# Optimization experiments

Hardware: AMD Instinct MI355X
Metric: run time of the kernel (lower is better)

The kernel has to match this reference:

```python
import jax, jax.numpy as jnp
import numpy as np

B, N, E, H, DEPTH = 2, 2048, 1024, 8, 12
D = E // H // 2  # head_dim = 64
LN_EPS = 1e-5


def setup_inputs() -> dict:
    key = jax.random.key(0)
    ks = jax.random.split(key, 10)
    w = lambda k: jax.random.normal(k, (E, E), jnp.float32) * (E ** -0.5)
    lp = lambda k: jax.random.normal(k, (D,), jnp.float32) * 0.1
    return {
        "x": jax.random.normal(ks[0], (B, N, E), jnp.float32),
        "Wq": w(ks[1]), "Wk": w(ks[2]), "Wv": w(ks[3]), "Wo": w(ks[4]),
        "lq1": lp(ks[5]), "lk1": lp(ks[6]), "lq2": lp(ks[7]), "lk2": lp(ks[8]),
        "ln_g": jnp.ones((2 * D,), jnp.float32),
        "ln_b": jnp.zeros((2 * D,), jnp.float32),
    }


def reference(x, Wq, Wk, Wv, Wo, lq1, lk1, lq2, lk2, ln_g, ln_b):
    b, n, e = x.shape
    lam_init = 0.8 - 0.6 * np.exp(-0.3 * DEPTH)  # lambda_init_fn(depth)
    # projections; split into 2H half-heads of dim D for q,k; H heads of dim 2D for v
    q = (x @ Wq).reshape(b, n, 2 * H, D).transpose(0, 2, 1, 3) * (D ** -0.5)  # [b,2H,n,D]
    k = (x @ Wk).reshape(b, n, 2 * H, D).transpose(0, 2, 1, 3)                # [b,2H,n,D]
    v = (x @ Wv).reshape(b, n, H, 2 * D).transpose(0, 2, 1, 3)                # [b,H,n,2D]
    scores = jnp.einsum('bhqd,bhkd->bhqk', q, k)                              # [b,2H,n,n]
    attn = jax.nn.softmax(scores, axis=-1).reshape(b, H, 2, n, n)
    lam = jnp.exp(jnp.sum(lq1 * lk1)) - jnp.exp(jnp.sum(lq2 * lk2)) + lam_init
    w_diff = attn[:, :, 0] - lam * attn[:, :, 1]                              # [b,H,n,n]
    o = jnp.einsum('bhqk,bhkd->bhqd', w_diff, v)                              # [b,H,n,2D]
    # per-head LayerNorm over channel dim 2D
    mu = o.mean(-1, keepdims=True)
    var = ((o - mu) ** 2).mean(-1, keepdims=True)
    o = (o - mu) * jax.lax.rsqrt(var + LN_EPS) * ln_g + ln_b
    o = o.transpose(0, 2, 1, 3).reshape(b, n, e)
    return o @ Wo
```

## Files before the change

### kernel.cpp

```cpp
#include <hip/hip_runtime.h>
#include <hip/hip_bf16.h>
#include <math.h>

#define B_ 2
#define N_ 2048
#define E_ 1024
#define H_ 8

typedef __attribute__((ext_vector_type(8))) short frag8;
typedef __attribute__((ext_vector_type(4))) float f32x4;
typedef __attribute__((ext_vector_type(16))) float f32x16;
typedef __attribute__((ext_vector_type(8))) unsigned short u16x8;

constexpr float LAM_INIT = 0.7836057665316245f;
constexpr float LOG2E = 1.4426950408889634f;
constexpr float EXP2_GUARD = -23.083120654f;

static __device__ __forceinline__ float fast_exp2(float x) {
#if __has_builtin(__builtin_amdgcn_exp2f)
  return __builtin_amdgcn_exp2f(x);
#else
  return exp2f(x);
#endif
}

static __device__ __forceinline__ ushort f2bf(float f) {
  union { float f; unsigned u; } v; v.f = f;
  unsigned r = (v.u + 0x7FFFu + ((v.u >> 16) & 1u)) >> 16;
  return (ushort)r;
}

static __device__ __forceinline__ unsigned pkbf(float a, float b) {
  __hip_bfloat162 h = __float22bfloat162_rn(make_float2(a, b));
  return *(unsigned*)&h;
}

static __device__ __forceinline__ float bf2f_lo(unsigned u) {
  union { unsigned u; float f; } v; v.u = u << 16; return v.f;
}
static __device__ __forceinline__ float bf2f_hi(unsigned u) {
  union { unsigned u; float f; } v; v.u = u & 0xFFFF0000u; return v.f;
}

static __device__ __forceinline__ void async16(const void* g, void* l) {
  __builtin_amdgcn_global_load_lds((const __attribute__((address_space(1))) void*)g,
                                   (__attribute__((address_space(3))) void*)l, 16, 0, 0);
}

static __device__ __forceinline__ frag8 mkfrag(unsigned p0, unsigned p1,
                                               unsigned p2, unsigned p3) {
  auto r02 = __builtin_amdgcn_permlane32_swap((int)p0, (int)p2, false, false);
  auto r13 = __builtin_amdgcn_permlane32_swap((int)p1, (int)p3, false, false);
  union { unsigned u[4]; frag8 f; } u;
  u.u[0] = (unsigned)r02[0];
  u.u[1] = (unsigned)r13[0];
  u.u[2] = (unsigned)r02[1];
  u.u[3] = (unsigned)r13[1];
  return u.f;
}

__global__ __launch_bounds__(256) void prep_kernel(
    const float* __restrict__ x,
    const float* __restrict__ Wq, const float* __restrict__ Wk,
    const float* __restrict__ Wv, const float* __restrict__ Wo,
    const float* __restrict__ lq1, const float* __restrict__ lk1,
    const float* __restrict__ lq2, const float* __restrict__ lk2,
    ushort* __restrict__ xb, ushort* __restrict__ wqkvt, ushort* __restrict__ wot,
    float* __restrict__ lam_out) {
  __shared__ ushort t[64][72];
  const int bx = blockIdx.x;
  const int tid = threadIdx.x;
  if (bx < 2048) {
    int i = bx * 256 + tid;
    const float4* sp = (const float4*)x + (size_t)i * 2;
    float4 a = sp[0], b = sp[1];
    u16x8 o;
    o[0] = f2bf(a.x); o[1] = f2bf(a.y); o[2] = f2bf(a.z); o[3] = f2bf(a.w);
    o[4] = f2bf(b.x); o[5] = f2bf(b.y); o[6] = f2bf(b.z); o[7] = f2bf(b.w);
    *(u16x8*)(xb + (size_t)i * 8) = o;
  } else if (bx < 3072) {
    int idx = bx - 2048;
    int sel = idx >> 8, rem = idx & 255;
    const float* W = (sel == 0) ? Wq : (sel == 1) ? Wk : (sel == 2) ? Wv : Wo;
    ushort* Wt = (sel < 3) ? (wqkvt + (size_t)sel * 1048576) : wot;
    const int c0 = (rem & 15) * 64, r0 = (rem >> 4) * 64;
    {
      int r = tid >> 2, cc = (tid & 3) * 16;
      const float* sp = W + (size_t)(r0 + r) * 1024 + c0 + cc;
      #pragma unroll
      for (int j = 0; j < 4; j++) {
        float4 a = *(const float4*)(sp + j * 4);
        t[cc + j * 4 + 0][r] = f2bf(a.x);
        t[cc + j * 4 + 1][r] = f2bf(a.y);
        t[cc + j * 4 + 2][r] = f2bf(a.z);
        t[cc + j * 4 + 3][r] = f2bf(a.w);
      }
    }
    __syncthreads();
    int c = tid >> 2, rr = (tid & 3) * 16;
    ushort* dp = Wt + (size_t)(c0 + c) * 1024 + r0 + rr;
    *(u16x8*)dp = *(u16x8*)&t[c][rr];
    *(u16x8*)(dp + 8) = *(u16x8*)&t[c][rr + 8];
  } else {
    if (tid < 64) {
      float t1 = lq1[tid] * lk1[tid];
      float t2 = lq2[tid] * lk2[tid];
      #pragma unroll
      for (int off = 32; off > 0; off >>= 1) {
        t1 += __shfl_down(t1, off);
        t2 += __shfl_down(t2, off);
      }
      if (tid == 0) lam_out[0] = expf(t1) - expf(t2) + LAM_INIT;
    }
  }
}

__global__ __launch_bounds__(256) void gemm_qkv(const ushort* __restrict__ xb,
                                                const ushort* __restrict__ wqkvt,
                                                ushort* __restrict__ qkb,
                                                ushort* __restrict__ vtb, float qscale) {
  __shared__ ushort As[4096];
  __shared__ ushort Bs[4096];
  const int id = blockIdx.x;
  const ushort* A; const ushort* Bt; ushort* C;
  int m0, n0, ldc;
  float sc;
  if (id < 512) {
    m0 = (id >> 4) * 128; n0 = (id & 15) * 128;
    A = xb; Bt = wqkvt; C = qkb; ldc = 2048;
    sc = (n0 < 1024) ? qscale : 1.0f;
  } else {
    int id2 = id - 512;
    m0 = (id2 & 7) * 128; n0 = (id2 >> 3) * 128;
    A = wqkvt + 2 * 1048576; Bt = xb; C = vtb; ldc = 4096;
    sc = 1.0f;
  }
  const int tid = threadIdx.x;
  const int w = tid >> 6, l = tid & 63;
  const int quad = l >> 4, col16 = l & 15;
  const int wm = (w & 1) * 64, wn = (w >> 1) * 64;
  const int lrow = l >> 2, lcol = (l & 3) * 8;

  f32x4 acc[4][4];
  #pragma unroll
  for (int mt = 0; mt < 4; mt++)
    #pragma unroll
    for (int nt = 0; nt < 4; nt++) acc[mt][nt] = (f32x4){0.f, 0.f, 0.f, 0.f};

  for (int k0 = 0; k0 < 1024; k0 += 32) {
    __syncthreads();
    #pragma unroll
    for (int i = 0; i < 4; i++) {
      int s = w * 4 + i;
      if (s < 8) {
        const ushort* gp = A + (size_t)(m0 + s * 16 + lrow) * 1024 + k0 + lcol;
        async16(gp, (char*)As + s * 1024);
      } else {
        int s2 = s - 8;
        const ushort* gp = Bt + (size_t)(n0 + s2 * 16 + lrow) * 1024 + k0 + lcol;
        async16(gp, (char*)Bs + s2 * 1024);
      }
    }
    __syncthreads();
    frag8 af[4], bfr[4];
    #pragma unroll
    for (int mt = 0; mt < 4; mt++)
      af[mt] = *(const frag8*)((const char*)As + (wm + mt * 16 + col16) * 64 + quad * 16);
    #pragma unroll
    for (int nt = 0; nt < 4; nt++)
      bfr[nt] = *(const frag8*)((const char*)Bs + (wn + nt * 16 + col16) * 64 + quad * 16);
    #pragma unroll
    for (int mt = 0; mt < 4; mt++)
      #pragma unroll
      for (int nt = 0; nt < 4; nt++)
        acc[mt][nt] = __builtin_amdgcn_mfma_f32_16x16x32_bf16(af[mt], bfr[nt], acc[mt][nt], 0, 0, 0);
  }

  #pragma unroll
  for (int mt = 0; mt < 4; mt++)
    #pragma unroll
    for (int r = 0; r < 4; r++) {
      int m = m0 + wm + mt * 16 + quad * 4 + r;
      #pragma unroll
      for (int nt = 0; nt < 4; nt++) {
        int n = n0 + wn + nt * 16 + col16;
        C[(size_t)m * ldc + n] = f2bf(acc[mt][nt][r] * sc);
      }
    }
}

__global__ __launch_bounds__(256) void gemm_out(const ushort* __restrict__ A,
                                                const ushort* __restrict__ Bt,
                                                float* __restrict__ Cp) {
  __shared__ ushort As[2048];
  __shared__ ushort Bs[4096];
  const int tid = threadIdx.x;
  const int w = tid >> 6, l = tid & 63;
  const int quad = l >> 4, col16 = l & 15;
  const int m0 = blockIdx.y * 64, n0 = blockIdx.x * 128;
  const int wm = (w & 1) * 32, wn = (w >> 1) * 64;
  const int lrow = l >> 2, lcol = (l & 3) * 8;

  f32x4 acc[2][4];
  #pragma unroll
  for (int mt = 0; mt < 2; mt++)
    #pragma unroll
    for (int nt = 0; nt < 4; nt++) acc[mt][nt] = (f32x4){0.f, 0.f, 0.f, 0.f};

  for (int k0 = 0; k0 < 1024; k0 += 32) {
    __syncthreads();
    #pragma unroll
    for (int i = 0; i < 3; i++) {
      int s = w * 3 + i;
      if (s < 4) {
        const ushort* gp = A + (size_t)(m0 + s * 16 + lrow) * 1024 + k0 + lcol;
        async16(gp, (char*)As + s * 1024);
      } else {
        int s2 = s - 4;
        const ushort* gp = Bt + (size_t)(n0 + s2 * 16 + lrow) * 1024 + k0 + lcol;
        async16(gp, (char*)Bs + s2 * 1024);
      }
    }
    __syncthreads();
    frag8 af[2], bfr[4];
    #pragma unroll
    for (int mt = 0; mt < 2; mt++)
      af[mt] = *(const frag8*)((const char*)As + (wm + mt * 16 + col16) * 64 + quad * 16);
    #pragma unroll
    for (int nt = 0; nt < 4; nt++)
      bfr[nt] = *(const frag8*)((const char*)Bs + (wn + nt * 16 + col16) * 64 + quad * 16);
    #pragma unroll
    for (int mt = 0; mt < 2; mt++)
      #pragma unroll
      for (int nt = 0; nt < 4; nt++)
        acc[mt][nt] = __builtin_amdgcn_mfma_f32_16x16x32_bf16(af[mt], bfr[nt], acc[mt][nt], 0, 0, 0);
  }

  #pragma unroll
  for (int mt = 0; mt < 2; mt++)
    #pragma unroll
    for (int r = 0; r < 4; r++) {
      int m = m0 + wm + mt * 16 + quad * 4 + r;
      #pragma unroll
      for (int nt = 0; nt < 4; nt++) {
        int n = n0 + wn + nt * 16 + col16;
        Cp[(size_t)m * 1024 + n] = acc[mt][nt][r];
      }
    }
}

__global__ __launch_bounds__(256, 2) void flash_kernel(const ushort* __restrict__ qk,
                                                       const ushort* __restrict__ vt,
                                                       ushort* __restrict__ opart,
                                                       float* __restrict__ lbuf) {
  const int h2 = blockIdx.y;
  const int b = blockIdx.z;
  const int h = h2 >> 1;
  const int tid = threadIdx.x;
  const int w = tid >> 6;
  const int lane31 = tid & 31, half = (tid & 63) >> 5;
  const int i0 = blockIdx.x * 128 + w * 32;

  __shared__ ushort Klds0[64 * 64], Klds1[64 * 64];
  __shared__ ushort Vlds0[128 * 64], Vlds1[128 * 64];

  frag8 qf[4];
  #pragma unroll
  for (int chk = 0; chk < 4; chk++) {
    const ushort* qp = qk + (size_t)(b * N_ + i0 + lane31) * 2048 +
                       h2 * 64 + chk * 16 + half * 8;
    qf[chk] = *(const frag8*)qp;
  }

  f32x16 o_[4];
  #pragma unroll
  for (int cm = 0; cm < 4; cm++)
    #pragma unroll
    for (int i = 0; i < 16; i++) o_[cm][i] = 0.f;
  float la0 = 0.f, la1 = 0.f;

  auto stage = [&](int k0, ushort* Kb, ushort* Vb) {
    #pragma unroll
    for (int it = 0; it < 2; it++) {
      int j = it * 256 + tid;
      int row = j >> 3, sch = (j & 7) ^ (row & 7);
      const ushort* kg = qk + (size_t)(b * N_ + k0 + row) * 2048 + 1024 + h2 * 64 + sch * 8;
      async16(kg, (char*)Kb + it * 4096 + w * 1024);
    }
    #pragma unroll
    for (int it = 0; it < 4; it++) {
      int j = it * 256 + tid;
      int row = j >> 3, sch = (j & 7) ^ (row & 7);
      const ushort* vg = vt + (size_t)(h * 128 + row) * 4096 + b * N_ + k0 + sch * 8;
      async16(vg, (char*)Vb + it * 4096 + w * 1024);
    }
  };

  auto compute = [&](const ushort* Kb, const ushort* Vb) {
    #pragma unroll
    for (int kh = 0; kh < 2; kh++) {
      f32x16 st;
      #pragma unroll
      for (int i = 0; i < 16; i++) st[i] = EXP2_GUARD;
      const int r = kh * 32 + lane31;
      #pragma unroll
      for (int chk = 0; chk < 4; chk++) {
        frag8 a = *(const frag8*)((const char*)Kb + r * 128 +
                                  (((chk << 1) | half) ^ (r & 7)) * 16);
        st = __builtin_amdgcn_mfma_f32_32x32x16_bf16(a, qf[chk], st, 0, 0, 0);
      }
      unsigned pk[8];
      #pragma unroll
      for (int p = 0; p < 8; p++) {
        float e0 = fast_exp2(st[2 * p]);
        float e1 = fast_exp2(st[2 * p + 1]);
        la0 += e0;
        la1 += e1;
        pk[p] = pkbf(e0, e1);
      }
      #pragma unroll
      for (int c16 = 0; c16 < 2; c16++) {
        frag8 bfr = mkfrag(pk[c16 * 4 + 0], pk[c16 * 4 + 1],
                           pk[c16 * 4 + 2], pk[c16 * 4 + 3]);
        #pragma unroll
        for (int cm = 0; cm < 4; cm++) {
          int c = cm * 32 + lane31;
          int g = (kh * 4 + c16 * 2 + half) ^ (c & 7);
          frag8 a = *(const frag8*)((const char*)Vb + c * 128 + g * 16);
          o_[cm] = __builtin_amdgcn_mfma_f32_32x32x16_bf16(a, bfr, o_[cm], 0, 0, 0);
        }
      }
    }
  };

  stage(0, Klds0, Vlds0);
  #pragma unroll 1
  for (int kt2 = 0; kt2 < 16; kt2++) {
    const int k0 = kt2 * 128;
    __syncthreads();
    stage(k0 + 64, Klds1, Vlds1);
    compute(Klds0, Vlds0);
    __syncthreads();
    if (kt2 < 15)
      stage(k0 + 128, Klds0, Vlds0);
    compute(Klds1, Vlds1);
  }

  float l_acc = la0 + la1;
  float lt = l_acc + __shfl_xor(l_acc, 32);
  if (half == 0)
    lbuf[(size_t)(b * 16 + h2) * N_ + i0 + lane31] = lt;

  {
    int q = i0 + lane31;
    ushort* ob = opart + ((size_t)((b * 16 + h2) * N_ + q)) * 128;
    #pragma unroll
    for (int cm = 0; cm < 4; cm++)
      #pragma unroll
      for (int g = 0; g < 4; g++) {
        int c = cm * 32 + g * 8 + half * 4;
        uint2 pv;
        pv.x = pkbf(o_[cm][4 * g + 0], o_[cm][4 * g + 1]);
        pv.y = pkbf(o_[cm][4 * g + 2], o_[cm][4 * g + 3]);
        *(uint2*)(ob + c) = pv;
      }
  }
}

__global__ __launch_bounds__(256) void combine_ln_kernel(
    const ushort* __restrict__ opart, const float* __restrict__ lbuf,
    const float* __restrict__ lam_p,
    const float* __restrict__ ln_g, const float* __restrict__ ln_b,
    ushort* __restrict__ onorm) {
  const float lam = lam_p[0];
  const int wave = threadIdx.x >> 6, lane = threadIdx.x & 63;
  const int row = blockIdx.x * 4 + wave;
  const int n = row & (N_ - 1);
  const int bh = row >> 11;
  const int h = bh & (H_ - 1);
  const int b = bh >> 3;

  const size_t re = (size_t)(b * 16 + 2 * h) * N_ + n;
  const size_t ro = (size_t)(b * 16 + 2 * h + 1) * N_ + n;
  const float rle = 1.0f / lbuf[re];
  const float rlo = 1.0f / lbuf[ro];

  const int c = lane * 2;
  unsigned e0 = *(const unsigned*)(opart + re * 128 + c);
  unsigned q0 = *(const unsigned*)(opart + ro * 128 + c);
  float ve0 = bf2f_lo(e0) * rle;
  float ve1 = bf2f_hi(e0) * rle;
  float vo0 = bf2f_lo(q0) * rlo;
  float vo1 = bf2f_hi(q0) * rlo;
  float v0 = ve0 - lam * vo0;
  float v1 = ve1 - lam * vo1;
  float sum = v0 + v1, ss = v0 * v0 + v1 * v1;
  #pragma unroll
  for (int off = 1; off < 64; off <<= 1) {
    sum += __shfl_xor(sum, off);
    ss += __shfl_xor(ss, off);
  }
  float mu = sum * (1.0f / 128.0f);
  float var = ss * (1.0f / 128.0f) - mu * mu;
  float r = rsqrtf(var + 1e-5f);
  float o0 = (v0 - mu) * r * ln_g[c] + ln_b[c];
  float o1 = (v1 - mu) * r * ln_g[c + 1] + ln_b[c + 1];
  unsigned pkv = (unsigned)f2bf(o0) | ((unsigned)f2bf(o1) << 16);
  *(unsigned*)(onorm + ((size_t)(b * N_ + n)) * E_ + h * 128 + c) = pkv;
}

extern "C" void kernel_launch(void* const* d_in, const int* in_sizes, int n_in,
                              void* d_out, int out_size, void* d_ws, size_t ws_size,
                              hipStream_t stream) {
  const float* x    = (const float*)d_in[0];
  const float* Wq   = (const float*)d_in[1];
  const float* Wk   = (const float*)d_in[2];
  const float* Wv   = (const float*)d_in[3];
  const float* Wo   = (const float*)d_in[4];
  const float* lq1  = (const float*)d_in[5];
  const float* lk1  = (const float*)d_in[6];
  const float* lq2  = (const float*)d_in[7];
  const float* lk2  = (const float*)d_in[8];
  const float* ln_g = (const float*)d_in[9];
  const float* ln_b = (const float*)d_in[10];
  float* out = (float*)d_out;

  const size_t MN = (size_t)B_ * N_ * E_;
  ushort* xb    = (ushort*)d_ws;
  ushort* wqkvt = xb + MN;
  ushort* wot   = wqkvt + 3 * 1048576;
  ushort* qkb   = wot + 1048576;
  ushort* vtb   = qkb + (size_t)4096 * 2048;
  ushort* op    = vtb + MN;
  float*  lbuf  = (float*)(op + 2 * MN);
  float*  lam   = lbuf + 65536;
  ushort* onorm = xb;

  prep_kernel<<<dim3(3073), 256, 0, stream>>>(x, Wq, Wk, Wv, Wo, lq1, lk1, lq2, lk2,
                                              xb, wqkvt, wot, lam);

  gemm_qkv<<<dim3(768), 256, 0, stream>>>(xb, wqkvt, qkb, vtb, 0.125f * LOG2E);

  flash_kernel<<<dim3(N_ / 128, 16, B_), 256, 0, stream>>>(qkb, vtb, op, lbuf);
  combine_ln_kernel<<<dim3(B_ * H_ * N_ / 4), 256, 0, stream>>>(op, lbuf, lam, ln_g, ln_b, onorm);
  gemm_out<<<dim3(8, 64), 256, 0, stream>>>(onorm, wot, out);
}
```

Measured before the change: 219.7 us.

## Load V fragments directly from global memory instead of staging through LDS

The flash attention kernel stops staging the V tile into double-buffered shared memory and instead has each lane load its V MFMA operand fragments straight from global (L2) memory for each 32-key half-tile. This removes the V async copies and the LDS reads, and cuts shared memory per block, which may allow more resident blocks. In exchange, the four waves in a block (and blocks sharing a head) each fetch V separately from global/L2, and those loads are not overlapped through the async pipeline, so their latency sits on the critical path before the PV MFMAs.

```diff
diff --git a/kernel.cpp b/kernel.cpp
--- a/kernel.cpp
+++ b/kernel.cpp
@@ -262,7 +262,8 @@
   const int i0 = blockIdx.x * 128 + w * 32;
 
   __shared__ ushort Klds0[64 * 64], Klds1[64 * 64];
-  __shared__ ushort Vlds0[128 * 64], Vlds1[128 * 64];
+
+  const ushort* vbase = vt + (size_t)(h * 128 + lane31) * 4096 + b * N_ + half * 8;
 
   frag8 qf[4];
   #pragma unroll
@@ -279,7 +280,7 @@
     for (int i = 0; i < 16; i++) o_[cm][i] = 0.f;
   float la0 = 0.f, la1 = 0.f;
 
-  auto stage = [&](int k0, ushort* Kb, ushort* Vb) {
+  auto stage = [&](int k0, ushort* Kb) {
     #pragma unroll
     for (int it = 0; it < 2; it++) {
       int j = it * 256 + tid;
@@ -287,18 +288,18 @@
       const ushort* kg = qk + (size_t)(b * N_ + k0 + row) * 2048 + 1024 + h2 * 64 + sch * 8;
       async16(kg, (char*)Kb + it * 4096 + w * 1024);
     }
-    #pragma unroll
-    for (int it = 0; it < 4; it++) {
-      int j = it * 256 + tid;
-      int row = j >> 3, sch = (j & 7) ^ (row & 7);
-      const ushort* vg = vt + (size_t)(h * 128 + row) * 4096 + b * N_ + k0 + sch * 8;
-      async16(vg, (char*)Vb + it * 4096 + w * 1024);
-    }
   };
 
-  auto compute = [&](const ushort* Kb, const ushort* Vb) {
+  auto compute = [&](const ushort* Kb, int k0) {
     #pragma unroll
     for (int kh = 0; kh < 2; kh++) {
+      frag8 vf0[4], vf1[4];
+      #pragma unroll
+      for (int cm = 0; cm < 4; cm++) {
+        const ushort* vg = vbase + (size_t)cm * (32 * 4096) + k0 + kh * 32;
+        vf0[cm] = *(const frag8*)vg;
+        vf1[cm] = *(const frag8*)(vg + 16);
+      }
       f32x16 st;
       #pragma unroll
       for (int i = 0; i < 16; i++) st[i] = EXP2_GUARD;
@@ -318,32 +319,32 @@
         la1 += e1;
         pk[p] = pkbf(e0, e1);
       }
-      #pragma unroll
-      for (int c16 = 0; c16 < 2; c16++) {
-        frag8 bfr = mkfrag(pk[c16 * 4 + 0], pk[c16 * 4 + 1],
-                           pk[c16 * 4 + 2], pk[c16 * 4 + 3]);
+      {
+        frag8 bfr = mkfrag(pk[0], pk[1], pk[2], pk[3]);
         #pragma unroll
-        for (int cm = 0; cm < 4; cm++) {
-          int c = cm * 32 + lane31;
-          int g = (kh * 4 + c16 * 2 + half) ^ (c & 7);
-          frag8 a = *(const frag8*)((const char*)Vb + c * 128 + g * 16);
-          o_[cm] = __builtin_amdgcn_mfma_f32_32x32x16_bf16(a, bfr, o_[cm], 0, 0, 0);
-        }
+        for (int cm = 0; cm < 4; cm++)
+          o_[cm] = __builtin_amdgcn_mfma_f32_32x32x16_bf16(vf0[cm], bfr, o_[cm], 0, 0, 0);
+      }
+      {
+        frag8 bfr = mkfrag(pk[4], pk[5], pk[6], pk[7]);
+        #pragma unroll
+        for (int cm = 0; cm < 4; cm++)
+          o_[cm] = __builtin_amdgcn_mfma_f32_32x32x16_bf16(vf1[cm], bfr, o_[cm], 0, 0, 0);
       }
     }
   };
 
-  stage(0, Klds0, Vlds0);
+  stage(0, Klds0);
   #pragma unroll 1
   for (int kt2 = 0; kt2 < 16; kt2++) {
     const int k0 = kt2 * 128;
     __syncthreads();
-    stage(k0 + 64, Klds1, Vlds1);
-    compute(Klds0, Vlds0);
+    stage(k0 + 64, Klds1);
+    compute(Klds0, k0);
     __syncthreads();
     if (kt2 < 15)
-      stage(k0 + 128, Klds0, Vlds0);
-    compute(Klds1, Vlds1);
+      stage(k0 + 128, Klds0);
+    compute(Klds1, k0 + 64);
   }
 
   float l_acc = la0 + la1;
```

New measurement: 288.1 us. +31.1%, slower.

## Fuse differential combine and LayerNorm into flash kernel with paired half-heads per block

Applied to the files above, without the earlier changes.

Each flash block now runs 512 threads covering both half-heads of one head for the same 128 query rows. The two halves share the staged V tile, and the odd half passes its unnormalized output and row sums through LDS so the even half can apply the lambda difference and LayerNorm and write bf16 directly. This removes the separate combine kernel and the global round trip of partial outputs and row sums, and halves V loads. It also adds s_setprio around the MFMA sections. The cost is a much larger LDS footprint (64KB of staging plus a 64KB fp32 epilogue buffer) that may cut occupancy, and only half the waves do work during the epilogue.

```diff
diff --git a/kernel.cpp b/kernel.cpp
--- a/kernel.cpp
+++ b/kernel.cpp
@@ -249,20 +249,30 @@
     }
 }
 
-__global__ __launch_bounds__(256, 2) void flash_kernel(const ushort* __restrict__ qk,
+__global__ __launch_bounds__(512, 2) void flash_kernel(const ushort* __restrict__ qk,
                                                        const ushort* __restrict__ vt,
-                                                       ushort* __restrict__ opart,
-                                                       float* __restrict__ lbuf) {
-  const int h2 = blockIdx.y;
-  const int b = blockIdx.z;
-  const int h = h2 >> 1;
+                                                       const float* __restrict__ lam_p,
+                                                       const float* __restrict__ ln_g,
+                                                       const float* __restrict__ ln_b,
+                                                       ushort* __restrict__ onorm) {
+  const int L = blockIdx.x;
+  const int hb = (L & 7) | (((L >> 3) & 1) << 3);
+  const int qb = L >> 4;
+  const int h = hb & 7, b = hb >> 3;
+
   const int tid = threadIdx.x;
   const int w = tid >> 6;
+  const int hsel = w >> 2;
+  const int h2 = 2 * h + hsel;
   const int lane31 = tid & 31, half = (tid & 63) >> 5;
-  const int i0 = blockIdx.x * 128 + w * 32;
-
-  __shared__ ushort Klds0[64 * 64], Klds1[64 * 64];
-  __shared__ ushort Vlds0[128 * 64], Vlds1[128 * 64];
+  const int qloc = (w & 3) * 32 + lane31;
+  const int i0 = qb * 128 + (w & 3) * 32;
+
+  __shared__ char bufA[32768], bufB[32768];
+  __shared__ float epi[128 * 128];
+  __shared__ float epi_l[128];
+
+  const float lam = lam_p[0];
 
   frag8 qf[4];
   #pragma unroll
@@ -279,36 +289,42 @@
     for (int i = 0; i < 16; i++) o_[cm][i] = 0.f;
   float la0 = 0.f, la1 = 0.f;
 
-  auto stage = [&](int k0, ushort* Kb, ushort* Vb) {
+  auto stage = [&](int k0, char* buf) {
+    {
+      int row = tid >> 3, sch = (tid & 7) ^ (row & 7);
+      const ushort* kg = qk + (size_t)(b * N_ + k0 + row) * 2048 + 1024 + (2 * h) * 64 + sch * 8;
+      async16(kg, buf + w * 1024);
+    }
+    {
+      int row = tid >> 3, sch = (tid & 7) ^ (row & 7);
+      const ushort* kg = qk + (size_t)(b * N_ + k0 + row) * 2048 + 1024 + (2 * h + 1) * 64 + sch * 8;
+      async16(kg, buf + 8192 + w * 1024);
+    }
     #pragma unroll
     for (int it = 0; it < 2; it++) {
-      int j = it * 256 + tid;
-      int row = j >> 3, sch = (j & 7) ^ (row & 7);
-      const ushort* kg = qk + (size_t)(b * N_ + k0 + row) * 2048 + 1024 + h2 * 64 + sch * 8;
-      async16(kg, (char*)Kb + it * 4096 + w * 1024);
-    }
-    #pragma unroll
-    for (int it = 0; it < 4; it++) {
-      int j = it * 256 + tid;
+      int j = it * 512 + tid;
       int row = j >> 3, sch = (j & 7) ^ (row & 7);
       const ushort* vg = vt + (size_t)(h * 128 + row) * 4096 + b * N_ + k0 + sch * 8;
-      async16(vg, (char*)Vb + it * 4096 + w * 1024);
+      async16(vg, buf + 16384 + it * 8192 + w * 1024);
     }
   };
 
-  auto compute = [&](const ushort* Kb, const ushort* Vb) {
+  auto compute = [&](const char* buf) {
+    const char* Kb = buf + hsel * 8192;
+    const char* Vb = buf + 16384;
     #pragma unroll
     for (int kh = 0; kh < 2; kh++) {
       f32x16 st;
       #pragma unroll
       for (int i = 0; i < 16; i++) st[i] = EXP2_GUARD;
       const int r = kh * 32 + lane31;
+      __builtin_amdgcn_s_setprio(1);
       #pragma unroll
       for (int chk = 0; chk < 4; chk++) {
-        frag8 a = *(const frag8*)((const char*)Kb + r * 128 +
-                                  (((chk << 1) | half) ^ (r & 7)) * 16);
+        frag8 a = *(const frag8*)(Kb + r * 128 + (((chk << 1) | half) ^ (r & 7)) * 16);
         st = __builtin_amdgcn_mfma_f32_32x32x16_bf16(a, qf[chk], st, 0, 0, 0);
       }
+      __builtin_amdgcn_s_setprio(0);
       unsigned pk[8];
       #pragma unroll
       for (int p = 0; p < 8; p++) {
@@ -322,91 +338,92 @@
       for (int c16 = 0; c16 < 2; c16++) {
         frag8 bfr = mkfrag(pk[c16 * 4 + 0], pk[c16 * 4 + 1],
                            pk[c16 * 4 + 2], pk[c16 * 4 + 3]);
+        __builtin_amdgcn_s_setprio(1);
         #pragma unroll
         for (int cm = 0; cm < 4; cm++) {
           int c = cm * 32 + lane31;
           int g = (kh * 4 + c16 * 2 + half) ^ (c & 7);
-          frag8 a = *(const frag8*)((const char*)Vb + c * 128 + g * 16);
+          frag8 a = *(const frag8*)(Vb + c * 128 + g * 16);
           o_[cm] = __builtin_amdgcn_mfma_f32_32x32x16_bf16(a, bfr, o_[cm], 0, 0, 0);
         }
+        __builtin_amdgcn_s_setprio(0);
       }
     }
   };
 
-  stage(0, Klds0, Vlds0);
+  stage(0, bufA);
   #pragma unroll 1
   for (int kt2 = 0; kt2 < 16; kt2++) {
     const int k0 = kt2 * 128;
     __syncthreads();
-    stage(k0 + 64, Klds1, Vlds1);
-    compute(Klds0, Vlds0);
+    stage(k0 + 64, bufB);
+    compute(bufA);
     __syncthreads();
     if (kt2 < 15)
-      stage(k0 + 128, Klds0, Vlds0);
-    compute(Klds1, Vlds1);
+      stage(k0 + 128, bufA);
+    compute(bufB);
   }
 
   float l_acc = la0 + la1;
   float lt = l_acc + __shfl_xor(l_acc, 32);
-  if (half == 0)
-    lbuf[(size_t)(b * 16 + h2) * N_ + i0 + lane31] = lt;
-
-  {
-    int q = i0 + lane31;
-    ushort* ob = opart + ((size_t)((b * 16 + h2) * N_ + q)) * 128;
+
+  if (hsel == 1) {
+    if (half == 0) epi_l[qloc] = lt;
     #pragma unroll
     for (int cm = 0; cm < 4; cm++)
       #pragma unroll
       for (int g = 0; g < 4; g++) {
         int c = cm * 32 + g * 8 + half * 4;
+        int pch = (c >> 2) ^ (qloc & 31);
+        *(f32x4*)&epi[qloc * 128 + pch * 4] =
+            (f32x4){o_[cm][4 * g + 0], o_[cm][4 * g + 1],
+                    o_[cm][4 * g + 2], o_[cm][4 * g + 3]};
+      }
+  }
+  __syncthreads();
+  if (hsel == 0) {
+    const float rle = 1.0f / lt;
+    const float rlo = 1.0f / epi_l[qloc];
+    float sum = 0.f, ss = 0.f;
+    #pragma unroll
+    for (int cm = 0; cm < 4; cm++)
+      #pragma unroll
+      for (int g = 0; g < 4; g++) {
+        int c = cm * 32 + g * 8 + half * 4;
+        int pch = (c >> 2) ^ (qloc & 31);
+        f32x4 ov = *(const f32x4*)&epi[qloc * 128 + pch * 4];
+        #pragma unroll
+        for (int j = 0; j < 4; j++) {
+          float v = o_[cm][4 * g + j] * rle - lam * ov[j] * rlo;
+          o_[cm][4 * g + j] = v;
+          sum += v;
+          ss += v * v;
+        }
+      }
+    sum += __shfl_xor(sum, 32);
+    ss += __shfl_xor(ss, 32);
+    float mu = sum * (1.0f / 128.0f);
+    float var = ss * (1.0f / 128.0f) - mu * mu;
+    float rr = rsqrtf(var + 1e-5f);
+    int q = qb * 128 + qloc;
+    ushort* ob = onorm + ((size_t)(b * N_ + q)) * E_ + h * 128;
+    #pragma unroll
+    for (int cm = 0; cm < 4; cm++)
+      #pragma unroll
+      for (int g = 0; g < 4; g++) {
+        int c = cm * 32 + g * 8 + half * 4;
+        float4 g4 = *(const float4*)&ln_g[c];
+        float4 b4 = *(const float4*)&ln_b[c];
+        float v0 = (o_[cm][4 * g + 0] - mu) * rr * g4.x + b4.x;
+        float v1 = (o_[cm][4 * g + 1] - mu) * rr * g4.y + b4.y;
+        float v2 = (o_[cm][4 * g + 2] - mu) * rr * g4.z + b4.z;
+        float v3 = (o_[cm][4 * g + 3] - mu) * rr * g4.w + b4.w;
         uint2 pv;
-        pv.x = pkbf(o_[cm][4 * g + 0], o_[cm][4 * g + 1]);
-        pv.y = pkbf(o_[cm][4 * g + 2], o_[cm][4 * g + 3]);
+        pv.x = pkbf(v0, v1);
+        pv.y = pkbf(v2, v3);
         *(uint2*)(ob + c) = pv;
       }
   }
-}
-
-__global__ __launch_bounds__(256) void combine_ln_kernel(
-    const ushort* __restrict__ opart, const float* __restrict__ lbuf,
-    const float* __restrict__ lam_p,
-    const float* __restrict__ ln_g, const float* __restrict__ ln_b,
-    ushort* __restrict__ onorm) {
-  const float lam = lam_p[0];
-  const int wave = threadIdx.x >> 6, lane = threadIdx.x & 63;
-  const int row = blockIdx.x * 4 + wave;
-  const int n = row & (N_ - 1);
-  const int bh = row >> 11;
-  const int h = bh & (H_ - 1);
-  const int b = bh >> 3;
-
-  const size_t re = (size_t)(b * 16 + 2 * h) * N_ + n;
-  const size_t ro = (size_t)(b * 16 + 2 * h + 1) * N_ + n;
-  const float rle = 1.0f / lbuf[re];
-  const float rlo = 1.0f / lbuf[ro];
-
-  const int c = lane * 2;
-  unsigned e0 = *(const unsigned*)(opart + re * 128 + c);
-  unsigned q0 = *(const unsigned*)(opart + ro * 128 + c);
-  float ve0 = bf2f_lo(e0) * rle;
-  float ve1 = bf2f_hi(e0) * rle;
-  float vo0 = bf2f_lo(q0) * rlo;
-  float vo1 = bf2f_hi(q0) * rlo;
-  float v0 = ve0 - lam * vo0;
-  float v1 = ve1 - lam * vo1;
-  float sum = v0 + v1, ss = v0 * v0 + v1 * v1;
-  #pragma unroll
-  for (int off = 1; off < 64; off <<= 1) {
-    sum += __shfl_xor(sum, off);
-    ss += __shfl_xor(ss, off);
-  }
-  float mu = sum * (1.0f / 128.0f);
-  float var = ss * (1.0f / 128.0f) - mu * mu;
-  float r = rsqrtf(var + 1e-5f);
-  float o0 = (v0 - mu) * r * ln_g[c] + ln_b[c];
-  float o1 = (v1 - mu) * r * ln_g[c + 1] + ln_b[c + 1];
-  unsigned pkv = (unsigned)f2bf(o0) | ((unsigned)f2bf(o1) << 16);
-  *(unsigned*)(onorm + ((size_t)(b * N_ + n)) * E_ + h * 128 + c) = pkv;
 }
 
 extern "C" void kernel_launch(void* const* d_in, const int* in_sizes, int n_in,
@@ -431,9 +448,7 @@
   ushort* wot   = wqkvt + 3 * 1048576;
   ushort* qkb   = wot + 1048576;
   ushort* vtb   = qkb + (size_t)4096 * 2048;
-  ushort* op    = vtb + MN;
-  float*  lbuf  = (float*)(op + 2 * MN);
-  float*  lam   = lbuf + 65536;
+  float*  lam   = (float*)(vtb + MN);
   ushort* onorm = xb;
 
   prep_kernel<<<dim3(3073), 256, 0, stream>>>(x, Wq, Wk, Wv, Wo, lq1, lk1, lq2, lk2,
@@ -441,7 +456,7 @@
 
   gemm_qkv<<<dim3(768), 256, 0, stream>>>(xb, wqkvt, qkb, vtb, 0.125f * LOG2E);
 
-  flash_kernel<<<dim3(N_ / 128, 16, B_), 256, 0, stream>>>(qkb, vtb, op, lbuf);
-  combine_ln_kernel<<<dim3(B_ * H_ * N_ / 4), 256, 0, stream>>>(op, lbuf, lam, ln_g, ln_b, onorm);
+  flash_kernel<<<dim3(256), 512, 0, stream>>>(qkb, vtb, lam, ln_g, ln_b, onorm);
+
   gemm_out<<<dim3(8, 64), 256, 0, stream>>>(onorm, wot, out);
 }
```

Result: faster. 211.4 us (-3.8%).
